# Optimization experiments

Hardware: AMD Instinct MI355X
Metric: run time of the kernel (lower is better)

The kernel has to match this reference:

```python
import jax, jax.numpy as jnp
import numpy as np

B = 16384
NUM_V = 1024
NUM_H = 1024
HYPER_DIM = 64
K = 10  # gibbs steps
T = 1.0


def setup_inputs() -> dict:
    key = jax.random.key(0)
    ks = jax.random.split(key, 9)
    v_data = jax.random.bernoulli(ks[0], 0.5, (B, NUM_V)).astype(jnp.float32)
    cond = jax.random.uniform(ks[1], (B, 1), jnp.float32)
    W = 0.01 * jax.random.normal(ks[2], (NUM_V, NUM_H), jnp.float32)
    b = 0.01 * jax.random.normal(ks[3], (NUM_V,), jnp.float32)
    c = 0.01 * jax.random.normal(ks[4], (NUM_H,), jnp.float32)
    fc1_w = jax.random.normal(ks[5], (HYPER_DIM, 1), jnp.float32)
    fc1_b = jnp.zeros((HYPER_DIM,), jnp.float32)
    fc2_w = jax.random.normal(ks[6], (2 * (NUM_V + NUM_H), HYPER_DIM), jnp.float32) / np.sqrt(HYPER_DIM)
    fc2_b = jnp.zeros((2 * (NUM_V + NUM_H),), jnp.float32)
    return {"v_data": v_data, "cond": cond, "W": W, "b": b, "c": c,
            "fc1_w": fc1_w, "fc1_b": fc1_b, "fc2_w": fc2_w, "fc2_b": fc2_b}


def _mod_biases(cond, b, c, fc1_w, fc1_b, fc2_w, fc2_b):
    x = jnp.tanh(cond @ fc1_w.T + fc1_b)
    y = x @ fc2_w.T + fc2_b  # [B, 2*(num_v+num_h)]
    gamma_b, beta_b, gamma_c, beta_c = jnp.split(
        y, [NUM_V, 2 * NUM_V, 2 * NUM_V + NUM_H], axis=-1)
    b_mod = (1.0 + gamma_b) * b[None, :] + beta_b  # [B, num_v]
    c_mod = (1.0 + gamma_c) * c[None, :] + beta_c  # [B, num_h]
    return b_mod, c_mod


def _free_energy(v, W, b_mod, c_mod):
    vW = v @ W  # [B, num_h]
    W_colsum = W.sum(axis=0)  # [num_h]
    sp_normal = jax.nn.softplus(vW + c_mod).sum(axis=-1)
    sp_flipped = jax.nn.softplus(W_colsum[None, :] - vW + c_mod).sum(axis=-1)
    vb_normal = -(v * b_mod).sum(axis=-1)
    vb_flipped = -((1.0 - v) * b_mod).sum(axis=-1)
    F_normal = vb_normal - sp_normal
    F_flipped = vb_flipped - sp_flipped
    negF = jnp.stack([-F_normal, -F_flipped], axis=-1)
    return -T * jax.nn.logsumexp(negF / T, axis=-1)


def _gibbs_step(carry, step_key, W, b_mod, c_mod):
    v, u = carry
    kh, ku, kv = jax.random.split(step_key, 3)
    v_branch = u * v + (1.0 - u) * (1.0 - v)
    p_h = jax.nn.sigmoid((v_branch @ W + c_mod) / T)
    h = jax.random.bernoulli(kh, p_h).astype(v.dtype)
    a = h @ W.T  # [B, num_v]
    dE = (-b_mod.sum(axis=-1) - a.sum(axis=-1)
          + 2.0 * (v * b_mod).sum(axis=-1) + 2.0 * (v * a).sum(axis=-1))
    p_u = jax.nn.sigmoid(dE / T)
    u = jax.random.bernoulli(ku, p_u).astype(v.dtype)[:, None]
    p_v = jax.nn.sigmoid((a + b_mod) / T)
    v_branch_new = jax.random.bernoulli(kv, p_v).astype(v.dtype)
    v_next = u * v_branch_new + (1.0 - u) * (1.0 - v_branch_new)
    return (v_next, u), None


def reference(v_data, cond, W, b, c, fc1_w, fc1_b, fc2_w, fc2_b):
    b_mod, c_mod = _mod_biases(cond, b, c, fc1_w, fc1_b, fc2_w, fc2_b)
    Bn = v_data.shape[0]
    key = jax.random.key(42)
    k_u, k_chain = jax.random.split(key)
    u0 = jax.random.bernoulli(k_u, 0.5, (Bn, 1)).astype(v_data.dtype)
    step_keys = jax.random.split(k_chain, K)
    step = lambda carry, sk: _gibbs_step(carry, sk, W, b_mod, c_mod)
    (v_model, _), _ = jax.lax.scan(step, (v_data, u0), step_keys)
    v_model = jax.lax.stop_gradient(v_model)
    loss = (_free_energy(v_data, W, b_mod, c_mod).mean()
            - _free_energy(v_model, W, b_mod, c_mod).mean())
    return loss
```

## Files before the change

### kernel.cpp

```cpp
#include <hip/hip_runtime.h>
#include <hip/hip_bf16.h>
#include <stdint.h>


#define NB 16384
#define KSTEPS 10
#define LDA 1152
#define KD 1088
#define NT 17
#define SLS 136
#define USALT 4000u
#define BONE ((unsigned char)7)
#define PSC 0x1.0p-13f
#define RWQ 1170.2857142857f
#define SGQ 64.0f
#define SXQ 128.0f

typedef __attribute__((ext_vector_type(4))) float f32x4;
typedef __attribute__((ext_vector_type(4))) int i32x4;
typedef __attribute__((ext_vector_type(4))) unsigned int u32x4;

__device__ __forceinline__ unsigned hash32(unsigned idx, unsigned salt) {
  unsigned x = idx + salt * 0x9E3779B9u;
  x = (x ^ (x >> 16)) * 0x7feb352du;
  x = (x ^ (x >> 15)) * 0x846ca68bu;
  return x ^ (x >> 16);
}
__device__ __forceinline__ float rng_u01(unsigned salt, unsigned idx) {
  return (float)(hash32(idx, salt) >> 8) * (1.0f / 16777216.0f);
}
__device__ __forceinline__ float sigm(float z) { return 1.0f / (1.0f + __expf(-z)); }
__device__ __forceinline__ float softplus_(float z) {
  return fmaxf(z, 0.f) + __logf(1.f + __expf(-fabsf(z)));
}
__device__ __forceinline__ float lse2(float a, float b) {
  float m = fmaxf(a, b);
  return m + log1pf(__expf(fminf(a, b) - m));
}
__device__ __forceinline__ unsigned char qi8(float v, float s) {
  float x = rintf(v * s);
  x = fminf(fmaxf(x, -127.f), 127.f);
  return (unsigned char)(signed char)(int)x;
}
__device__ __forceinline__ void gl2lds16(const void* g, void* l) {
  __builtin_amdgcn_global_load_lds(
      (const __attribute__((address_space(1))) unsigned int*)g,
      (__attribute__((address_space(3))) unsigned int*)l, 16, 0, 0);
}

template <int EPI>
__global__ __launch_bounds__(256, 4) void gemm_bt(
    const unsigned char* __restrict__ A, const unsigned char* __restrict__ Bt,
    unsigned char* sh, const float* __restrict__ cst,
    const float* __restrict__ wcs, const float* __restrict__ Xf,
    const float* __restrict__ pv0, const float* __restrict__ pv1, unsigned usalt,
    float* __restrict__ p0, float* __restrict__ p1, float* __restrict__ p2,
    unsigned salt) {
  constexpr int MI = (EPI == 2 ? 2 : 4);
  constexpr int BM = MI * 32;
  constexpr int ABYT = BM * 64;
  constexpr int BUF = ABYT + 8192;
  __shared__ __align__(16) char smem[2 * BUF];
  unsigned char* newsl = (unsigned char*)smem;

  const int t = threadIdx.x;
  const int L = blockIdx.x;
  const int xcd = L & 7, li = L >> 3;
  constexpr int MMSK = (EPI == 2 ? 31 : 15);
  constexpr int NSH = (EPI == 2 ? 5 : 4);
  const int m0 = xcd * 2048 + (li & MMSK) * BM;
  const int n0 = (li >> NSH) * 128;
  const int lane = t & 63, wave = t >> 6;
  const int wm = (wave >> 1) * (MI * 16), wn = (wave & 1) * 64;
  const int lr = lane & 15, quad = lane >> 4;
  const int row8 = lane >> 2;
  const int qch = (((lane & 3) ^ (row8 & 3) ^ ((lane >> 4) & 3)) << 4);
  const int rx = (lr & 3) ^ ((lr >> 2) & 3);
  const int kph = ((quad ^ rx) << 4);

  const unsigned char* gA0 = A + (size_t)(m0 + wave * (MI * 8) + row8) * LDA + qch;
  const unsigned char* gA1 = gA0 + (size_t)16 * LDA;
  const unsigned char* gB0 = Bt + (size_t)(n0 + wave * 32 + row8) * LDA + qch;
  const unsigned char* gB1 = gB0 + (size_t)16 * LDA;

  auto stage = [&](int it, int bufb) {
    const int ko = it * 64;
    if constexpr (EPI == 2) {
      gl2lds16(gA0 + ko, smem + bufb + wave * 1024);
    } else {
      gl2lds16(gA0 + ko, smem + bufb + wave * 2048);
      gl2lds16(gA1 + ko, smem + bufb + wave * 2048 + 1024);
    }
    gl2lds16(gB0 + ko, smem + bufb + ABYT + wave * 2048);
    gl2lds16(gB1 + ko, smem + bufb + ABYT + wave * 2048 + 1024);
  };

  i32x4 acc[MI][4] = {};
  i32x4 accf[EPI == 2 ? MI : 1][4] = {};

  stage(0, 0);
  __syncthreads();

#pragma unroll
  for (int it = 0; it < NT; ++it) {
    const int base = (it & 1) * BUF;
    if (it + 1 < NT) stage(it + 1, base ^ BUF);
    const char* sA = (const char*)smem + base;
    const char* sB = sA + ABYT;
    i32x4 af[MI], bfr[4];
#pragma unroll
    for (int i = 0; i < MI; i++)
      af[i] = *(const i32x4*)(sA + (wm + i * 16 + lr) * 64 + kph);
#pragma unroll
    for (int j = 0; j < 4; j++)
      bfr[j] = *(const i32x4*)(sB + (wn + j * 16 + lr) * 64 + kph);
    if (EPI == 2 && it >= 16) {
#pragma unroll
      for (int i = 0; i < MI; i++)
#pragma unroll
        for (int j = 0; j < 4; j++)
          accf[i][j] = __builtin_amdgcn_mfma_i32_16x16x64_i8(af[i], bfr[j], accf[i][j], 0, 0, 0);
    } else {
#pragma unroll
      for (int i = 0; i < MI; i++)
#pragma unroll
        for (int j = 0; j < 4; j++)
          acc[i][j] = __builtin_amdgcn_mfma_i32_16x16x64_i8(af[i], bfr[j], acc[i][j], 0, 0, 0);
    }
    __syncthreads();
  }

  float cst_j[4];
  if constexpr (EPI != 2) {
#pragma unroll
    for (int j = 0; j < 4; j++) cst_j[j] = cst[n0 + wn + j * 16 + lr];
  }

  if constexpr (EPI == 2) {
    if (n0 >= 1024) {
#pragma unroll
      for (int i = 0; i < MI; i++)
#pragma unroll
        for (int rg = 0; rg < 4; rg++) {
          const int r = m0 + wm + i * 16 + quad * 4 + rg;
          float pb = 0.f;
          if (wn == 0) {
#pragma unroll
            for (int j = 0; j < 4; j++)
              pb += (float)acc[i][j][rg] * Xf[(size_t)r * 64 + j * 16 + lr];
            pb *= (1.f / 448.f);
          } else {
            if (lr == 0) pb = (float)acc[i][0][rg] * PSC;
          }
#pragma unroll
          for (int msk = 1; msk < 16; msk <<= 1) pb += __shfl_xor(pb, msk, 64);
          if (lr == 0) atomicAdd(&p2[r], pb);
        }
      return;
    }
    float cstc_j[4];
#pragma unroll
    for (int j = 0; j < 4; j++) cstc_j[j] = cst[n0 + wn + j * 16 + lr];
#pragma unroll
    for (int i = 0; i < MI; i++)
#pragma unroll
      for (int rg = 0; rg < 4; rg++) {
        const int r = m0 + wm + i * 16 + quad * 4 + rg;
        bool uu = true;
        if (pv0 != nullptr) {
          const float dE = -pv0[r] + 2.f * pv1[r];
          uu = rng_u01(usalt, (unsigned)r) < sigm(dE);
        }
        float sn = 0.f, sf = 0.f;
#pragma unroll
        for (int j = 0; j < 4; j++) {
          const int n = n0 + wn + j * 16 + lr;
          const float vw = (float)acc[i][j][rg] * PSC;
          const float cm = (float)accf[i][j][rg] * PSC + cstc_j[j];
          const float s1 = softplus_(vw + cm);
          const float s2 = softplus_(wcs[n] - vw + cm);
          sn += uu ? s1 : s2;
          sf += uu ? s2 : s1;
        }
#pragma unroll
        for (int msk = 1; msk < 16; msk <<= 1) {
          sn += __shfl_xor(sn, msk, 64);
          sf += __shfl_xor(sf, msk, 64);
        }
        if (lr == 0) { atomicAdd(&p0[r], sn); atomicAdd(&p1[r], sf); }
      }
    return;
  }

  if constexpr (EPI == 1) {
    {
      const int rb = wave * (MI * 8);
#pragma unroll
      for (int q = 0; q < MI; ++q) {
        const int row = rb + q * 8 + (lane >> 3);
        const int sc = (lane & 7) ^ ((row >> 2) & 3);
        gl2lds16(sh + (size_t)(m0 + row) * LDA + n0 + sc * 16,
                 (unsigned char*)smem + BUF + (rb + q * 8) * 128);
      }
    }
    __syncthreads();
    const unsigned char* osl = (const unsigned char*)smem + BUF;
#pragma unroll
    for (int i = 0; i < MI; i++)
#pragma unroll
      for (int rg = 0; rg < 4; rg++) {
        const int r = m0 + wm + i * 16 + quad * 4 + rg;
        const int rowl = wm + i * 16 + quad * 4 + rg;
        const float dE = -pv0[r] + 2.f * pv1[r];
        const bool uu = rng_u01(usalt, (unsigned)r) < sigm(dE);
        float q0 = 0.f, q1 = 0.f;
#pragma unroll
        for (int j = 0; j < 4; ++j) {
          const float z = (float)acc[i][j][rg] * PSC + cst_j[j];
          const int pc = ((wn >> 4) + j) ^ quad;
          const float so = (osl[rowl * 128 + pc * 16 + lr] != 0) ? 1.f : 0.f;
          const float v = uu ? so : 1.f - so;
          q0 += z; q1 += v * z;
        }
#pragma unroll
        for (int msk = 1; msk < 16; msk <<= 1) {
          q0 += __shfl_xor(q0, msk, 64);
          q1 += __shfl_xor(q1, msk, 64);
        }
        if (lr == 0) { atomicAdd(&p0[r], q0); atomicAdd(&p1[r], q1); }
      }
    __syncthreads();
  }

#pragma unroll
  for (int i = 0; i < MI; ++i)
#pragma unroll
    for (int rg = 0; rg < 4; ++rg) {
      const int rowl = wm + i * 16 + quad * 4 + rg;
      const int r = m0 + rowl;
#pragma unroll
      for (int jp = 0; jp < 2; ++jp) {
        const unsigned x = hash32((unsigned)(r << 10) + (unsigned)(n0 + wn + jp * 16 + lr), salt);
        const float f0 = (float)(x & 0xFFFFu), f1 = (float)(x >> 16);
        const float z0 = (float)acc[i][jp][rg] * PSC + cst_j[jp];
        const float z1v = (float)acc[i][jp + 2][rg] * PSC + cst_j[jp + 2];
        newsl[rowl * SLS + wn + jp * 16 + lr] =
            (f0 * __expf(-z0) < 65536.f - f0) ? BONE : (unsigned char)0;
        newsl[rowl * SLS + wn + (jp + 2) * 16 + lr] =
            (f1 * __expf(-z1v) < 65536.f - f1) ? BONE : (unsigned char)0;
      }
    }
  __syncthreads();
#pragma unroll
  for (int p = 0; p < BM / 32; ++p) {
    const int c = p * 256 + t, rowl = c >> 3, chk = c & 7;
    const u32x4 vv = *(const u32x4*)(newsl + rowl * SLS + chk * 16);
    *(u32x4*)(sh + (size_t)(m0 + rowl) * LDA + n0 + chk * 16) = vv;
  }
}

__global__ __launch_bounds__(256) void k_x(const float* __restrict__ cond,
                                           const float* __restrict__ fc1w,
                                           const float* __restrict__ fc1b, float* __restrict__ X) {
  int idx = blockIdx.x * 256 + threadIdx.x;
  int r = idx >> 6, k = idx & 63;
  X[idx] = tanhf(cond[r] * fc1w[k] + fc1b[k]);
}

__global__ __launch_bounds__(256) void k_g(const float* __restrict__ fc2w,
                                           const float* __restrict__ fc2b,
                                           const float* __restrict__ b, const float* __restrict__ c,
                                           float* __restrict__ Gb, float* __restrict__ Gc,
                                           float* __restrict__ cstb, float* __restrict__ cstc) {
  int idx = blockIdx.x * 256 + threadIdx.x;
  int j = idx >> 6, k = idx & 63;
  Gb[idx] = fc2w[(size_t)j * 64 + k] * b[j] + fc2w[(size_t)(1024 + j) * 64 + k];
  Gc[idx] = fc2w[(size_t)(2048 + j) * 64 + k] * c[j] + fc2w[(size_t)(3072 + j) * 64 + k];
  if (k == 0) {
    cstb[j] = b[j] + fc2b[j] * b[j] + fc2b[1024 + j];
    cstc[j] = c[j] + fc2b[2048 + j] * c[j] + fc2b[3072 + j];
  }
}

__global__ __launch_bounds__(256) void k_prep(const float* __restrict__ W,
                                              const float* __restrict__ Gb,
                                              const float* __restrict__ Gc,
                                              const float* __restrict__ cstb,
                                              const float* __restrict__ cstc,
                                              unsigned char* __restrict__ Wt,
                                              unsigned char* __restrict__ Wb) {
  int k = blockIdx.x * 256 + threadIdx.x;
  int n = blockIdx.y;
  if (k >= LDA) return;
  unsigned char wt = 0, wb = 0;
  if (n < 1024) {
    if (k < 1024) {
      wt = qi8(W[(size_t)k * 1024 + n], RWQ);
      wb = qi8(W[(size_t)n * 1024 + k], RWQ);
    } else if (k < 1088) {
      int j = k - 1024;
      wt = qi8(Gc[(size_t)n * 64 + j], SGQ);
      wb = qi8(Gb[(size_t)n * 64 + j], SGQ);
    } else if (k == 1088) {
      wt = qi8(cstc[n], RWQ);
      wb = qi8(cstb[n], RWQ);
    }
  } else if (k < 1024) {
    if (n < 1088) wt = qi8(Gb[(size_t)k * 64 + (n - 1024)], SGQ);
    else if (n == 1088) wt = qi8(cstb[k], RWQ);
  }
  Wt[(size_t)n * LDA + k] = wt;
  Wb[(size_t)n * LDA + k] = wb;
}

__global__ __launch_bounds__(256) void k_wcs(const float* __restrict__ W, float* __restrict__ wcs) {
  int n = blockIdx.x * 256 + threadIdx.x;
  float s = 0.f;
  for (int i = 0; i < 1024; i++) s += W[(size_t)i * 1024 + n];
  wcs[n] = s;
}

__global__ __launch_bounds__(128) void k_aux(const float* __restrict__ Gb,
                                             const float* __restrict__ cstb,
                                             float* __restrict__ aux) {
  int t = threadIdx.x;
  if (t < 64) {
    float s = 0.f;
    for (int j = 0; j < 1024; j++) s += Gb[(size_t)j * 64 + t];
    aux[t] = s;
  } else if (t == 64) {
    float s = 0.f;
    for (int j = 0; j < 1024; j++) s += cstb[j];
    aux[64] = s;
  }
}

__global__ __launch_bounds__(256) void k_sinit(const float* __restrict__ vdata,
                                               const float* __restrict__ X,
                                               unsigned char* __restrict__ S,
                                               unsigned char* __restrict__ H,
                                               unsigned char* __restrict__ V) {
  int k = blockIdx.x * 256 + threadIdx.x;
  int r = blockIdx.y;
  if (k >= LDA) return;
  const size_t o = (size_t)r * LDA + k;
  if (k < 1024) {
    float vd = vdata[(size_t)r * 1024 + k];
    V[o] = (vd != 0.f) ? BONE : (unsigned char)0;
    const bool u0 = rng_u01(USALT, (unsigned)r) < 0.5f;
    float sv = u0 ? vd : 1.f - vd;
    S[o] = (sv != 0.f) ? BONE : (unsigned char)0;
  } else {
    unsigned char xv = 0;
    if (k < 1088) xv = qi8(X[(size_t)r * 64 + (k - 1024)], SXQ);
    S[o] = xv; H[o] = xv; V[o] = xv;
  }
}

__global__ __launch_bounds__(256) void k_final(
    const float* __restrict__ Xf, const float* __restrict__ aux,
    const float* __restrict__ pv0, const float* __restrict__ pv1, unsigned usalt,
    const float* __restrict__ spn_d, const float* __restrict__ spf_d,
    const float* __restrict__ spn_m, const float* __restrict__ spf_m,
    const float* __restrict__ vb_d, const float* __restrict__ vb_m,
    float* __restrict__ fdiff) {
  __shared__ float ax[65];
  int t = threadIdx.x;
  if (t < 65) ax[t] = aux[t];
  __syncthreads();
  int r = blockIdx.x * 256 + t;
  float sb = ax[64];
  const float* xr = Xf + (size_t)r * 64;
#pragma unroll
  for (int k = 0; k < 64; k++) sb += xr[k] * ax[k];
  const float dE = -pv0[r] + 2.f * pv1[r];
  const bool uu = rng_u01(usalt, (unsigned)r) < sigm(dE);
  const float d1 = vb_d[r], d2 = vb_m[r];
  float F_d = -lse2(d1 + spn_d[r], (sb - d1) + spf_d[r]);
  float vbn = uu ? d2 : (sb - d2);
  float F_m = -lse2(vbn + spn_m[r], (sb - vbn) + spf_m[r]);
  fdiff[r] = F_d - F_m;
}

__global__ __launch_bounds__(256) void k_reduce(const float* __restrict__ fdiff,
                                                float* __restrict__ out) {
  __shared__ float red[4];
  int t = threadIdx.x;
  float s = 0.f;
  for (int i = t; i < NB; i += 256) s += fdiff[i];
  for (int m = 32; m >= 1; m >>= 1) s += __shfl_xor(s, m, 64);
  if ((t & 63) == 0) red[t >> 6] = s;
  __syncthreads();
  if (t == 0) out[0] = (red[0] + red[1] + red[2] + red[3]) * (1.0f / (float)NB);
}

extern "C" void kernel_launch(void* const* d_in, const int* in_sizes, int n_in, void* d_out,
                              int out_size, void* d_ws, size_t ws_size, hipStream_t stream) {
  const float* vdata = (const float*)d_in[0];
  const float* cond = (const float*)d_in[1];
  const float* W = (const float*)d_in[2];
  const float* bb = (const float*)d_in[3];
  const float* cc = (const float*)d_in[4];
  const float* fc1w = (const float*)d_in[5];
  const float* fc1b = (const float*)d_in[6];
  const float* fc2w = (const float*)d_in[7];
  const float* fc2b = (const float*)d_in[8];
  float* out = (float*)d_out;

  char* wp = (char*)d_ws;
  auto alloc = [&](size_t bytes) {
    char* p = wp;
    wp += (bytes + 255) & ~(size_t)255;
    return p;
  };
  unsigned char* Wt = (unsigned char*)alloc((size_t)1152 * LDA);
  unsigned char* Wb = (unsigned char*)alloc((size_t)1152 * LDA);
  float* wcs = (float*)alloc(1024 * 4);
  float* X = (float*)alloc((size_t)NB * 64 * 4);
  float* Gb = (float*)alloc((size_t)1024 * 64 * 4);
  float* Gc = (float*)alloc((size_t)1024 * 64 * 4);
  float* cstb = (float*)alloc(1024 * 4);
  float* cstc = (float*)alloc(1024 * 4);
  float* aux = (float*)alloc(65 * 4);
  unsigned char* S = (unsigned char*)alloc((size_t)NB * LDA);
  unsigned char* H = (unsigned char*)alloc((size_t)NB * LDA);
  unsigned char* V = (unsigned char*)alloc((size_t)NB * LDA);
  float* pall = (float*)alloc((size_t)(KSTEPS + 1 + 3) * 2 * NB * 4);
  float* spn_d = pall + (size_t)(KSTEPS + 1) * 2 * NB;
  float* spf_d = spn_d + NB;
  float* spn_m = spf_d + NB;
  float* spf_m = spn_m + NB;
  float* vb_d = spf_m + NB;
  float* vb_m = vb_d + NB;
  float* fdiff = (float*)alloc(NB * 4);
  auto P0 = [&](int t) { return pall + (size_t)(t + 1) * 2 * NB; };
  auto P1 = [&](int t) { return pall + (size_t)(t + 1) * 2 * NB + NB; };

  hipMemsetAsync(pall, 0, (size_t)(KSTEPS + 1 + 3) * 2 * NB * 4, stream);

  k_x<<<NB * 64 / 256, 256, 0, stream>>>(cond, fc1w, fc1b, X);
  k_g<<<1024 * 64 / 256, 256, 0, stream>>>(fc2w, fc2b, bb, cc, Gb, Gc, cstb, cstc);
  k_prep<<<dim3(5, 1152), 256, 0, stream>>>(W, Gb, Gc, cstb, cstc, Wt, Wb);
  k_wcs<<<4, 256, 0, stream>>>(W, wcs);
  k_aux<<<1, 128, 0, stream>>>(Gb, cstb, aux);
  k_sinit<<<dim3(5, NB), 256, 0, stream>>>(vdata, X, S, H, V);

  for (int step = 0; step < KSTEPS; ++step) {
    gemm_bt<0><<<1024, 256, 0, stream>>>(S, Wt, H, cstc, nullptr, nullptr,
                                         nullptr, nullptr, 0u, nullptr, nullptr, nullptr,
                                         2000u + (unsigned)step);
    gemm_bt<1><<<1024, 256, 0, stream>>>(H, Wb, S, cstb, nullptr, nullptr,
                                         P0(step - 1), P1(step - 1), USALT + (unsigned)step,
                                         P0(step), P1(step), nullptr,
                                         3000u + (unsigned)step);
  }

  gemm_bt<2><<<2304, 256, 0, stream>>>(V, Wt, nullptr, cstc, wcs, X, nullptr, nullptr, 0u,
                                       spn_d, spf_d, vb_d, 0u);
  gemm_bt<2><<<2304, 256, 0, stream>>>(S, Wt, nullptr, cstc, wcs, X,
                                       P0(KSTEPS - 1), P1(KSTEPS - 1), USALT + KSTEPS,
                                       spn_m, spf_m, vb_m, 0u);
  k_final<<<NB / 256, 256, 0, stream>>>(X, aux, P0(KSTEPS - 1), P1(KSTEPS - 1), USALT + KSTEPS,
                                        spn_d, spf_d, spn_m, spf_m, vb_d, vb_m, fdiff);
  k_reduce<<<1, 256, 0, stream>>>(fdiff, out);
}
```

Baseline: 1.003 ms.

## Store int8 operands in MFMA-fragment tiled layout and load directly from global

Operand matrices (S, H, V, Wt, Wb) are now stored in a pre-tiled layout where each 16x64 block is laid out exactly as an MFMA fragment, so each lane reads its 16 bytes contiguously from global memory. The GEMM drops LDS staging, double buffering and per-iteration barriers and loads fragments straight into registers, which removes the synchronisation and LDS traffic cost. The epilogues and prep kernels are rewritten to read and write the tiled format, and the padding column is dropped. The trade-off is that there is no cross-wave reuse through LDS, so every wave fetches its own fragments from cache, and the loads are no longer overlapped with compute by explicit prefetch.

```diff
diff --git a/kernel.cpp b/kernel.cpp
--- a/kernel.cpp
+++ b/kernel.cpp
@@ -5,7 +5,6 @@
 
 #define NB 16384
 #define KSTEPS 10
-#define LDA 1152
 #define KD 1088
 #define NT 17
 #define SLS 136
@@ -19,6 +18,11 @@
 typedef __attribute__((ext_vector_type(4))) float f32x4;
 typedef __attribute__((ext_vector_type(4))) int i32x4;
 typedef __attribute__((ext_vector_type(4))) unsigned int u32x4;
+
+__device__ __forceinline__ size_t tflat(int row, int k) {
+  return ((size_t)(row >> 4) * NT + (k >> 6)) * 1024 +
+         (((k >> 4) & 3) << 8) + ((row & 15) << 4) + (k & 15);
+}
 
 __device__ __forceinline__ unsigned hash32(unsigned idx, unsigned salt) {
   unsigned x = idx + salt * 0x9E3779B9u;
@@ -58,9 +62,8 @@
     unsigned salt) {
   constexpr int MI = (EPI == 2 ? 2 : 4);
   constexpr int BM = MI * 32;
-  constexpr int ABYT = BM * 64;
-  constexpr int BUF = ABYT + 8192;
-  __shared__ __align__(16) char smem[2 * BUF];
+  constexpr int SMB = (EPI == 2 ? 16 : BM * SLS);
+  __shared__ __align__(16) char smem[SMB];
   unsigned char* newsl = (unsigned char*)smem;
 
   const int t = threadIdx.x;
@@ -73,47 +76,22 @@
   const int lane = t & 63, wave = t >> 6;
   const int wm = (wave >> 1) * (MI * 16), wn = (wave & 1) * 64;
   const int lr = lane & 15, quad = lane >> 4;
-  const int row8 = lane >> 2;
-  const int qch = (((lane & 3) ^ (row8 & 3) ^ ((lane >> 4) & 3)) << 4);
-  const int rx = (lr & 3) ^ ((lr >> 2) & 3);
-  const int kph = ((quad ^ rx) << 4);
-
-  const unsigned char* gA0 = A + (size_t)(m0 + wave * (MI * 8) + row8) * LDA + qch;
-  const unsigned char* gA1 = gA0 + (size_t)16 * LDA;
-  const unsigned char* gB0 = Bt + (size_t)(n0 + wave * 32 + row8) * LDA + qch;
-  const unsigned char* gB1 = gB0 + (size_t)16 * LDA;
-
-  auto stage = [&](int it, int bufb) {
-    const int ko = it * 64;
-    if constexpr (EPI == 2) {
-      gl2lds16(gA0 + ko, smem + bufb + wave * 1024);
-    } else {
-      gl2lds16(gA0 + ko, smem + bufb + wave * 2048);
-      gl2lds16(gA1 + ko, smem + bufb + wave * 2048 + 1024);
-    }
-    gl2lds16(gB0 + ko, smem + bufb + ABYT + wave * 2048);
-    gl2lds16(gB1 + ko, smem + bufb + ABYT + wave * 2048 + 1024);
-  };
+
+  const unsigned char* pA = A + (size_t)((m0 + wm) >> 4) * (NT * 1024) + lane * 16;
+  const unsigned char* pB = Bt + (size_t)((n0 + wn) >> 4) * (NT * 1024) + lane * 16;
 
   i32x4 acc[MI][4] = {};
   i32x4 accf[EPI == 2 ? MI : 1][4] = {};
 
-  stage(0, 0);
-  __syncthreads();
-
 #pragma unroll
   for (int it = 0; it < NT; ++it) {
-    const int base = (it & 1) * BUF;
-    if (it + 1 < NT) stage(it + 1, base ^ BUF);
-    const char* sA = (const char*)smem + base;
-    const char* sB = sA + ABYT;
     i32x4 af[MI], bfr[4];
 #pragma unroll
     for (int i = 0; i < MI; i++)
-      af[i] = *(const i32x4*)(sA + (wm + i * 16 + lr) * 64 + kph);
+      af[i] = *(const i32x4*)(pA + ((size_t)(i * NT + it) << 10));
 #pragma unroll
     for (int j = 0; j < 4; j++)
-      bfr[j] = *(const i32x4*)(sB + (wn + j * 16 + lr) * 64 + kph);
+      bfr[j] = *(const i32x4*)(pB + ((size_t)(j * NT + it) << 10));
     if (EPI == 2 && it >= 16) {
 #pragma unroll
       for (int i = 0; i < MI; i++)
@@ -127,7 +105,6 @@
         for (int j = 0; j < 4; j++)
           acc[i][j] = __builtin_amdgcn_mfma_i32_16x16x64_i8(af[i], bfr[j], acc[i][j], 0, 0, 0);
     }
-    __syncthreads();
   }
 
   float cst_j[4];
@@ -194,31 +171,29 @@
 
   if constexpr (EPI == 1) {
     {
-      const int rb = wave * (MI * 8);
-#pragma unroll
-      for (int q = 0; q < MI; ++q) {
-        const int row = rb + q * 8 + (lane >> 3);
-        const int sc = (lane & 7) ^ ((row >> 2) & 3);
-        gl2lds16(sh + (size_t)(m0 + row) * LDA + n0 + sc * 16,
-                 (unsigned char*)smem + BUF + (rb + q * 8) * 128);
+#pragma unroll
+      for (int q = 0; q < 4; ++q) {
+        const int tt = wave * 4 + q, rtl = tt >> 1, ktl = tt & 1;
+        gl2lds16(sh + ((size_t)((m0 >> 4) + rtl) * NT + (n0 >> 6) + ktl) * 1024 + lane * 16,
+                 (unsigned char*)smem + tt * 1024);
       }
     }
     __syncthreads();
-    const unsigned char* osl = (const unsigned char*)smem + BUF;
+    const unsigned char* osl = (const unsigned char*)smem;
 #pragma unroll
     for (int i = 0; i < MI; i++)
 #pragma unroll
       for (int rg = 0; rg < 4; rg++) {
         const int r = m0 + wm + i * 16 + quad * 4 + rg;
-        const int rowl = wm + i * 16 + quad * 4 + rg;
         const float dE = -pv0[r] + 2.f * pv1[r];
         const bool uu = rng_u01(usalt, (unsigned)r) < sigm(dE);
         float q0 = 0.f, q1 = 0.f;
 #pragma unroll
         for (int j = 0; j < 4; ++j) {
           const float z = (float)acc[i][j][rg] * PSC + cst_j[j];
-          const int pc = ((wn >> 4) + j) ^ quad;
-          const float so = (osl[rowl * 128 + pc * 16 + lr] != 0) ? 1.f : 0.f;
+          const int ob = (((wm >> 4) + i) * 2 + (wn >> 6)) * 1024 +
+                         j * 256 + (quad * 4 + rg) * 16 + lr;
+          const float so = (osl[ob] != 0) ? 1.f : 0.f;
           const float v = uu ? so : 1.f - so;
           q0 += z; q1 += v * z;
         }
@@ -253,9 +228,12 @@
   __syncthreads();
 #pragma unroll
   for (int p = 0; p < BM / 32; ++p) {
-    const int c = p * 256 + t, rowl = c >> 3, chk = c & 7;
-    const u32x4 vv = *(const u32x4*)(newsl + rowl * SLS + chk * 16);
-    *(u32x4*)(sh + (size_t)(m0 + rowl) * LDA + n0 + chk * 16) = vv;
+    const int c = p * 256 + t;
+    const int tt = c >> 6, l2 = c & 63;
+    const int rtl = tt >> 1, ktl = tt & 1;
+    const int srow = rtl * 16 + (l2 & 15), scol = ktl * 64 + (l2 >> 4) * 16;
+    const u32x4 vv = *(const u32x4*)(newsl + srow * SLS + scol);
+    *(u32x4*)(sh + ((size_t)((m0 >> 4) + rtl) * NT + (n0 >> 6) + ktl) * 1024 + l2 * 16) = vv;
   }
 }
 
@@ -291,26 +269,24 @@
                                               unsigned char* __restrict__ Wb) {
   int k = blockIdx.x * 256 + threadIdx.x;
   int n = blockIdx.y;
-  if (k >= LDA) return;
+  if (k >= KD) return;
   unsigned char wt = 0, wb = 0;
   if (n < 1024) {
     if (k < 1024) {
       wt = qi8(W[(size_t)k * 1024 + n], RWQ);
       wb = qi8(W[(size_t)n * 1024 + k], RWQ);
-    } else if (k < 1088) {
+    } else {
       int j = k - 1024;
       wt = qi8(Gc[(size_t)n * 64 + j], SGQ);
       wb = qi8(Gb[(size_t)n * 64 + j], SGQ);
-    } else if (k == 1088) {
-      wt = qi8(cstc[n], RWQ);
-      wb = qi8(cstb[n], RWQ);
     }
   } else if (k < 1024) {
     if (n < 1088) wt = qi8(Gb[(size_t)k * 64 + (n - 1024)], SGQ);
     else if (n == 1088) wt = qi8(cstb[k], RWQ);
   }
-  Wt[(size_t)n * LDA + k] = wt;
-  Wb[(size_t)n * LDA + k] = wb;
+  const size_t off = tflat(n, k);
+  Wt[off] = wt;
+  Wb[off] = wb;
 }
 
 __global__ __launch_bounds__(256) void k_wcs(const float* __restrict__ W, float* __restrict__ wcs) {
@@ -342,8 +318,8 @@
                                                unsigned char* __restrict__ V) {
   int k = blockIdx.x * 256 + threadIdx.x;
   int r = blockIdx.y;
-  if (k >= LDA) return;
-  const size_t o = (size_t)r * LDA + k;
+  if (k >= KD) return;
+  const size_t o = tflat(r, k);
   if (k < 1024) {
     float vd = vdata[(size_t)r * 1024 + k];
     V[o] = (vd != 0.f) ? BONE : (unsigned char)0;
@@ -351,8 +327,7 @@
     float sv = u0 ? vd : 1.f - vd;
     S[o] = (sv != 0.f) ? BONE : (unsigned char)0;
   } else {
-    unsigned char xv = 0;
-    if (k < 1088) xv = qi8(X[(size_t)r * 64 + (k - 1024)], SXQ);
+    unsigned char xv = qi8(X[(size_t)r * 64 + (k - 1024)], SXQ);
     S[o] = xv; H[o] = xv; V[o] = xv;
   }
 }
@@ -413,8 +388,8 @@
     wp += (bytes + 255) & ~(size_t)255;
     return p;
   };
-  unsigned char* Wt = (unsigned char*)alloc((size_t)1152 * LDA);
-  unsigned char* Wb = (unsigned char*)alloc((size_t)1152 * LDA);
+  unsigned char* Wt = (unsigned char*)alloc((size_t)72 * NT * 1024);
+  unsigned char* Wb = (unsigned char*)alloc((size_t)72 * NT * 1024);
   float* wcs = (float*)alloc(1024 * 4);
   float* X = (float*)alloc((size_t)NB * 64 * 4);
   float* Gb = (float*)alloc((size_t)1024 * 64 * 4);
@@ -422,9 +397,9 @@
   float* cstb = (float*)alloc(1024 * 4);
   float* cstc = (float*)alloc(1024 * 4);
   float* aux = (float*)alloc(65 * 4);
-  unsigned char* S = (unsigned char*)alloc((size_t)NB * LDA);
-  unsigned char* H = (unsigned char*)alloc((size_t)NB * LDA);
-  unsigned char* V = (unsigned char*)alloc((size_t)NB * LDA);
+  unsigned char* S = (unsigned char*)alloc((size_t)(NB / 16) * NT * 1024);
+  unsigned char* H = (unsigned char*)alloc((size_t)(NB / 16) * NT * 1024);
+  unsigned char* V = (unsigned char*)alloc((size_t)(NB / 16) * NT * 1024);
   float* pall = (float*)alloc((size_t)(KSTEPS + 1 + 3) * 2 * NB * 4);
   float* spn_d = pall + (size_t)(KSTEPS + 1) * 2 * NB;
   float* spf_d = spn_d + NB;
```

Result: slower. 1.211 ms (+20.7%).
